# Optimization experiments

Measured on AMD Instinct MI355X. Metric: run time of the kernel, lower is better.

## Reference

```python
import jax, jax.numpy as jnp
import numpy as np


def setup_inputs() -> dict:
    key = jax.random.key(0)
    k1, k2 = jax.random.split(key)
    N, K, D = 262144, 1024, 64
    x = jax.random.normal(k1, (N, D), dtype=jnp.float32)
    # nn.Embedding init: uniform(-1/num_embeddings, 1/num_embeddings)
    codebook = jax.random.uniform(k2, (K, D), dtype=jnp.float32,
                                  minval=-1.0 / K, maxval=1.0 / K)
    return {"x": x, "codebook": codebook}


def reference(x, codebook):
    # dis_mat[n,k] = ||x_n||^2 + ||e_k||^2 - 2 x_n . e_k  (squared L2)
    x_norm = jnp.sum(x * x, axis=1, keepdims=True)            # (N, 1)
    e_norm = jnp.sum(codebook * codebook, axis=1)             # (K,)
    dis_mat = x_norm + e_norm - 2.0 * (x @ codebook.T)        # (N, K)
    embed_inds = jnp.argmin(dis_mat, axis=1)                  # (N,)
    x_quantized = codebook[embed_inds]                        # (N, D) gather
    # compute_loss in the source is `pass` -> loss is None; omitted here.
    return x_quantized, embed_inds
```

## Files before the change

kernel.cpp:

```cpp
#include <hip/hip_runtime.h>
#include <float.h>


static constexpr int D_DIM = 64;
static constexpr int K_CB  = 1024;
static constexpr int TPB   = 256;
static constexpr int BM    = 128;
static constexpr int BN    = 128;
static constexpr int NKT   = K_CB / BN;
static constexpr int XS    = 68;

#define NP_INIT(c0, c1)                                                     \
    float ax = __fmul_rn(c0.x, c0.x), ay = __fmul_rn(c0.y, c0.y),           \
          az = __fmul_rn(c0.z, c0.z), aw = __fmul_rn(c0.w, c0.w);           \
    float bx = __fmul_rn(c1.x, c1.x), by = __fmul_rn(c1.y, c1.y),           \
          bz = __fmul_rn(c1.z, c1.z), bw = __fmul_rn(c1.w, c1.w);
#define NP_ACC(ce, co)                                                      \
    ax = __fadd_rn(ax, __fmul_rn(ce.x, ce.x));                              \
    ay = __fadd_rn(ay, __fmul_rn(ce.y, ce.y));                              \
    az = __fadd_rn(az, __fmul_rn(ce.z, ce.z));                              \
    aw = __fadd_rn(aw, __fmul_rn(ce.w, ce.w));                              \
    bx = __fadd_rn(bx, __fmul_rn(co.x, co.x));                              \
    by = __fadd_rn(by, __fmul_rn(co.y, co.y));                              \
    bz = __fadd_rn(bz, __fmul_rn(co.z, co.z));                              \
    bw = __fadd_rn(bw, __fmul_rn(co.w, co.w));
#define NP_TREE()                                                           \
    __fadd_rn(__fadd_rn(__fadd_rn(ax, ay), __fadd_rn(az, aw)),              \
              __fadd_rn(__fadd_rn(bx, by), __fadd_rn(bz, bw)))

__device__ __forceinline__ float np_pair_sq16(
        float4 c0, float4 c1, float4 c2, float4 c3,
        float4 c4, float4 c5, float4 c6, float4 c7,
        float4 c8, float4 c9, float4 c10, float4 c11,
        float4 c12, float4 c13, float4 c14, float4 c15) {
    NP_INIT(c0, c1)
    NP_ACC(c2, c3)  NP_ACC(c4, c5)  NP_ACC(c6, c7)
    NP_ACC(c8, c9)  NP_ACC(c10, c11) NP_ACC(c12, c13) NP_ACC(c14, c15)
    return NP_TREE();
}

__global__ void __launch_bounds__(TPB)
__attribute__((amdgpu_waves_per_eu(2, 2)))
vq_kernel(
        const float* __restrict__ x, const float* __restrict__ cb,
        float* __restrict__ out_q, float* __restrict__ out_idx) {
    __shared__ float xs[BM * XS];
    __shared__ float cs[BN * XS];
    __shared__ float es[K_CB];
    __shared__ float xn_s[BM];
    __shared__ int   bks[BM];

    const int tid = threadIdx.x;
    const int tx  = tid & 15;
    const int ty  = tid >> 4;
    const size_t row0 = (size_t)blockIdx.x * BM;
    const float4* cb4 = reinterpret_cast<const float4*>(cb);

#pragma unroll
    for (int j = 0; j < K_CB / TPB; ++j) {
        const int k = tid + TPB * j;
        const float4* cr = cb4 + (size_t)k * 16;
        float4 c0 = cr[0],  c1 = cr[1],  c2 = cr[2],  c3 = cr[3],
               c4 = cr[4],  c5 = cr[5],  c6 = cr[6],  c7 = cr[7],
               c8 = cr[8],  c9 = cr[9],  c10 = cr[10], c11 = cr[11],
               c12 = cr[12], c13 = cr[13], c14 = cr[14], c15 = cr[15];
        es[k] = np_pair_sq16(c0, c1, c2, c3, c4, c5, c6, c7,
                             c8, c9, c10, c11, c12, c13, c14, c15);
    }

    {
        const float4* g = reinterpret_cast<const float4*>(x + row0 * D_DIM);
#pragma unroll
        for (int j = 0; j < BM * 16 / TPB; ++j) {
            const int f = tid + TPB * j;
            const int r = f >> 4, c = f & 15;
            *reinterpret_cast<float4*>(&xs[r * XS + c * 4]) = g[f];
        }
    }
    __syncthreads();

    if (tid < BM) {
        const float* rp = &xs[tid * XS];
        float4 c0 = *(const float4*)&rp[0],  c1 = *(const float4*)&rp[4],
               c2 = *(const float4*)&rp[8],  c3 = *(const float4*)&rp[12],
               c4 = *(const float4*)&rp[16], c5 = *(const float4*)&rp[20],
               c6 = *(const float4*)&rp[24], c7 = *(const float4*)&rp[28],
               c8 = *(const float4*)&rp[32], c9 = *(const float4*)&rp[36],
               c10 = *(const float4*)&rp[40], c11 = *(const float4*)&rp[44],
               c12 = *(const float4*)&rp[48], c13 = *(const float4*)&rp[52],
               c14 = *(const float4*)&rp[56], c15 = *(const float4*)&rp[60];
        xn_s[tid] = np_pair_sq16(c0, c1, c2, c3, c4, c5, c6, c7,
                                 c8, c9, c10, c11, c12, c13, c14, c15);
    }
    __syncthreads();

    float xn[8];
#pragma unroll
    for (int i = 0; i < 8; ++i) xn[i] = xn_s[ty + 16 * i];

    float best[8]; int bestk[8];
#pragma unroll
    for (int i = 0; i < 8; ++i) { best[i] = FLT_MAX; bestk[i] = 0; }

    for (int t = 0; t < NKT; ++t) {
        __syncthreads();
        {
            const float4* g = cb4 + (size_t)t * BN * 16;
#pragma unroll
            for (int j = 0; j < BN * 16 / TPB; ++j) {
                const int f = tid + TPB * j;
                const int r = f >> 4, c = f & 15;
                *reinterpret_cast<float4*>(&cs[r * XS + c * 4]) = g[f];
            }
        }
        __syncthreads();

        float acc[8][8];
#pragma unroll
        for (int i = 0; i < 8; ++i)
#pragma unroll
            for (int j = 0; j < 8; ++j) acc[i][j] = 0.f;

#pragma unroll 2
        for (int dc = 0; dc < 16; ++dc) {
            float4 cq[8];
#pragma unroll
            for (int j = 0; j < 8; ++j)
                cq[j] = *(const float4*)&cs[(tx + 16 * j) * XS + dc * 4];
            float4 xq[4];
#pragma unroll
            for (int i = 0; i < 4; ++i)
                xq[i] = *(const float4*)&xs[(ty + 16 * i) * XS + dc * 4];
#pragma unroll
            for (int i = 0; i < 4; ++i)
#pragma unroll
                for (int j = 0; j < 8; ++j) {
                    acc[i][j] = __fmaf_rn(xq[i].x, cq[j].x, acc[i][j]);
                    acc[i][j] = __fmaf_rn(xq[i].y, cq[j].y, acc[i][j]);
                    acc[i][j] = __fmaf_rn(xq[i].z, cq[j].z, acc[i][j]);
                    acc[i][j] = __fmaf_rn(xq[i].w, cq[j].w, acc[i][j]);
                }
#pragma unroll
            for (int i = 0; i < 4; ++i)
                xq[i] = *(const float4*)&xs[(ty + 16 * (i + 4)) * XS + dc * 4];
#pragma unroll
            for (int i = 0; i < 4; ++i)
#pragma unroll
                for (int j = 0; j < 8; ++j) {
                    acc[i + 4][j] = __fmaf_rn(xq[i].x, cq[j].x, acc[i + 4][j]);
                    acc[i + 4][j] = __fmaf_rn(xq[i].y, cq[j].y, acc[i + 4][j]);
                    acc[i + 4][j] = __fmaf_rn(xq[i].z, cq[j].z, acc[i + 4][j]);
                    acc[i + 4][j] = __fmaf_rn(xq[i].w, cq[j].w, acc[i + 4][j]);
                }
        }

#pragma unroll
        for (int j = 0; j < 8; ++j) {
            const int k = t * BN + tx + 16 * j;
            const float en = es[k];
#pragma unroll
            for (int i = 0; i < 8; ++i) {
                const float s = __fmaf_rn(-2.f, acc[i][j], __fadd_rn(xn[i], en));
                if (s < best[i]) { best[i] = s; bestk[i] = k; }
            }
        }
    }

#pragma unroll
    for (int i = 0; i < 8; ++i) {
        float b = best[i]; int bk = bestk[i];
#pragma unroll
        for (int m = 1; m < 16; m <<= 1) {
            const float b2 = __shfl_xor(b, m);
            const int   k2 = __shfl_xor(bk, m);
            if (b2 < b || (b2 == b && k2 < bk)) { b = b2; bk = k2; }
        }
        if (tx == 0) {
            const int r = ty + 16 * i;
            bks[r] = bk;
            out_idx[row0 + r] = (float)bk;
        }
    }
    __syncthreads();

    float4* oq = reinterpret_cast<float4*>(out_q + row0 * D_DIM);
#pragma unroll
    for (int j = 0; j < BM * 16 / TPB; ++j) {
        const int f = tid + TPB * j;
        const int r = f >> 4, c = f & 15;
        oq[f] = cb4[(size_t)bks[r] * 16 + c];
    }
}

extern "C" void kernel_launch(void* const* d_in, const int* in_sizes, int n_in,
                              void* d_out, int out_size, void* d_ws, size_t ws_size,
                              hipStream_t stream) {
    const float* x  = (const float*)d_in[0];
    const float* cb = (const float*)d_in[1];
    const int n_rows = in_sizes[0] / D_DIM;

    float* out_q   = (float*)d_out;
    float* out_idx = out_q + (size_t)n_rows * D_DIM;

    vq_kernel<<<n_rows / BM, TPB, 0, stream>>>(x, cb, out_q, out_idx);
}
```

Baseline: 487.1 us.

## Widen codebook tile to 256 with 8x16 per-thread micro-tile and split-D staging

Doubles the codebook tile per iteration to 256 entries, so each thread accumulates an 8x16 block instead of 8x8. The tile is loaded in two halves along D, with a narrower padded stride, to keep shared memory near its previous size. The goal is more FMAs per LDS load and fewer tile iterations and barriers per codebook pass. In exchange, 128 accumulators plus operands raise register pressure under the 2-waves-per-EU bound, which risks spills, and each tile now needs an extra barrier for its second half.

```diff
diff --git a/kernel.cpp b/kernel.cpp
--- a/kernel.cpp
+++ b/kernel.cpp
@@ -6,9 +6,10 @@
 static constexpr int K_CB  = 1024;
 static constexpr int TPB   = 256;
 static constexpr int BM    = 128;
-static constexpr int BN    = 128;
+static constexpr int BN    = 256;
 static constexpr int NKT   = K_CB / BN;
 static constexpr int XS    = 68;
+static constexpr int CS    = 34;
 
 #define NP_INIT(c0, c1)                                                     \
     float ax = __fmul_rn(c0.x, c0.x), ay = __fmul_rn(c0.y, c0.y),           \
@@ -45,7 +46,7 @@
         const float* __restrict__ x, const float* __restrict__ cb,
         float* __restrict__ out_q, float* __restrict__ out_idx) {
     __shared__ float xs[BM * XS];
-    __shared__ float cs[BN * XS];
+    __shared__ float cs[BN * CS];
     __shared__ float es[K_CB];
     __shared__ float xn_s[BM];
     __shared__ int   bks[BM];
@@ -103,59 +104,56 @@
     for (int i = 0; i < 8; ++i) { best[i] = FLT_MAX; bestk[i] = 0; }
 
     for (int t = 0; t < NKT; ++t) {
-        __syncthreads();
-        {
-            const float4* g = cb4 + (size_t)t * BN * 16;
-#pragma unroll
-            for (int j = 0; j < BN * 16 / TPB; ++j) {
-                const int f = tid + TPB * j;
-                const int r = f >> 4, c = f & 15;
-                *reinterpret_cast<float4*>(&cs[r * XS + c * 4]) = g[f];
+        float acc[8][16];
+#pragma unroll
+        for (int i = 0; i < 8; ++i)
+#pragma unroll
+            for (int j = 0; j < 16; ++j) acc[i][j] = 0.f;
+
+#pragma unroll
+        for (int half = 0; half < 2; ++half) {
+            __syncthreads();
+            {
+                const int base = (t * BN) * 16 + half * 8;
+#pragma unroll
+                for (int jj = 0; jj < 8; ++jj) {
+                    const int f = tid + TPB * jj;
+                    const int r = f >> 3, c = f & 7;
+                    *reinterpret_cast<float4*>(&cs[r * CS + c * 4]) =
+                        cb4[(size_t)base + r * 16 + c];
+                }
             }
-        }
-        __syncthreads();
-
-        float acc[8][8];
-#pragma unroll
-        for (int i = 0; i < 8; ++i)
-#pragma unroll
-            for (int j = 0; j < 8; ++j) acc[i][j] = 0.f;
+            __syncthreads();
 
 #pragma unroll 2
-        for (int dc = 0; dc < 16; ++dc) {
-            float4 cq[8];
-#pragma unroll
-            for (int j = 0; j < 8; ++j)
-                cq[j] = *(const float4*)&cs[(tx + 16 * j) * XS + dc * 4];
-            float4 xq[4];
-#pragma unroll
-            for (int i = 0; i < 4; ++i)
-                xq[i] = *(const float4*)&xs[(ty + 16 * i) * XS + dc * 4];
-#pragma unroll
-            for (int i = 0; i < 4; ++i)
-#pragma unroll
-                for (int j = 0; j < 8; ++j) {
-                    acc[i][j] = __fmaf_rn(xq[i].x, cq[j].x, acc[i][j]);
-                    acc[i][j] = __fmaf_rn(xq[i].y, cq[j].y, acc[i][j]);
-                    acc[i][j] = __fmaf_rn(xq[i].z, cq[j].z, acc[i][j]);
-                    acc[i][j] = __fmaf_rn(xq[i].w, cq[j].w, acc[i][j]);
+            for (int dcl = 0; dcl < 8; ++dcl) {
+                const int dc = half * 8 + dcl;
+                float4 xq[8];
+#pragma unroll
+                for (int i = 0; i < 8; ++i)
+                    xq[i] = *(const float4*)&xs[(ty + 16 * i) * XS + dc * 4];
+#pragma unroll
+                for (int cg = 0; cg < 2; ++cg) {
+                    float4 cq[8];
+#pragma unroll
+                    for (int jj = 0; jj < 8; ++jj)
+                        cq[jj] = *(const float4*)&cs[(tx + 16 * (cg * 8 + jj)) * CS + dcl * 4];
+#pragma unroll
+                    for (int i = 0; i < 8; ++i)
+#pragma unroll
+                        for (int jj = 0; jj < 8; ++jj) {
+                            const int j = cg * 8 + jj;
+                            acc[i][j] = __fmaf_rn(xq[i].x, cq[jj].x, acc[i][j]);
+                            acc[i][j] = __fmaf_rn(xq[i].y, cq[jj].y, acc[i][j]);
+                            acc[i][j] = __fmaf_rn(xq[i].z, cq[jj].z, acc[i][j]);
+                            acc[i][j] = __fmaf_rn(xq[i].w, cq[jj].w, acc[i][j]);
+                        }
                 }
-#pragma unroll
-            for (int i = 0; i < 4; ++i)
-                xq[i] = *(const float4*)&xs[(ty + 16 * (i + 4)) * XS + dc * 4];
-#pragma unroll
-            for (int i = 0; i < 4; ++i)
-#pragma unroll
-                for (int j = 0; j < 8; ++j) {
-                    acc[i + 4][j] = __fmaf_rn(xq[i].x, cq[j].x, acc[i + 4][j]);
-                    acc[i + 4][j] = __fmaf_rn(xq[i].y, cq[j].y, acc[i + 4][j]);
-                    acc[i + 4][j] = __fmaf_rn(xq[i].z, cq[j].z, acc[i + 4][j]);
-                    acc[i + 4][j] = __fmaf_rn(xq[i].w, cq[j].w, acc[i + 4][j]);
-                }
-        }
-
-#pragma unroll
-        for (int j = 0; j < 8; ++j) {
+            }
+        }
+
+#pragma unroll
+        for (int j = 0; j < 16; ++j) {
             const int k = t * BN + tx + 16 * j;
             const float en = es[k];
 #pragma unroll
```

After: 508.5 us. 1.04x slower.
